# Optimization experiments

Measured on AMD Instinct MI355X. Metric: run time of the kernel, lower is better.

Reference implementation:

```python
import jax, jax.numpy as jnp
import numpy as np

D_MODEL = 1024
N_HEADS = 16
HEAD_DIM = D_MODEL // N_HEADS
ROPE_BASE = 10000.0


def setup_inputs() -> dict:
    key = jax.random.key(0)
    ks = jax.random.split(key, 9)
    s = 0.02
    inp = {
        "x": jax.random.normal(ks[0], (2, 2048, D_MODEL), dtype=jnp.float32),
        "Wq": jax.random.normal(ks[1], (D_MODEL, D_MODEL), dtype=jnp.float32) * s,
        "bq": jnp.zeros((D_MODEL,), dtype=jnp.float32),
        "Wk": jax.random.normal(ks[2], (D_MODEL, D_MODEL), dtype=jnp.float32) * s,
        "bk": jnp.zeros((D_MODEL,), dtype=jnp.float32),
        "Wv": jax.random.normal(ks[3], (D_MODEL, D_MODEL), dtype=jnp.float32) * s,
        "bv": jnp.zeros((D_MODEL,), dtype=jnp.float32),
        "Wo": jax.random.normal(ks[4], (D_MODEL, D_MODEL), dtype=jnp.float32) * s,
        "bo": jnp.zeros((D_MODEL,), dtype=jnp.float32),
    }
    return inp


def _rope_cos_sin(T, head_dim, dtype):
    inv_freq = 1.0 / (ROPE_BASE ** (jnp.arange(0, head_dim, 2, dtype=jnp.float32) / head_dim))
    pos = jnp.arange(T, dtype=jnp.float32)
    freqs = jnp.outer(pos, inv_freq)              # [T, head_dim/2]
    emb = jnp.concatenate([freqs, freqs], axis=-1)  # [T, head_dim]
    return jnp.cos(emb).astype(dtype), jnp.sin(emb).astype(dtype)


def _rotate_half(x):
    x1, x2 = jnp.split(x, 2, axis=-1)
    return jnp.concatenate([-x2, x1], axis=-1)


def reference(x, Wq, bq, Wk, bk, Wv, bv, Wo, bo):
    B, T, _ = x.shape
    H, Dh = N_HEADS, HEAD_DIM
    # projections (torch Linear: x @ W.T + b)
    q = (x @ Wq.T + bq).reshape(B, T, H, Dh).transpose(0, 2, 1, 3)  # [B,H,T,Dh]
    k = (x @ Wk.T + bk).reshape(B, T, H, Dh).transpose(0, 2, 1, 3)
    v = (x @ Wv.T + bv).reshape(B, T, H, Dh).transpose(0, 2, 1, 3)
    cos, sin = _rope_cos_sin(T, Dh, x.dtype)  # [T, Dh]
    cos = cos[None, None]
    sin = sin[None, None]
    q = q * cos + _rotate_half(q) * sin
    k = k * cos + _rotate_half(k) * sin
    scale = 1.0 / jnp.sqrt(jnp.asarray(Dh, dtype=x.dtype))
    attn = jnp.einsum("bhqd,bhkd->bhqk", q, k) * scale
    attn = jax.nn.softmax(attn, axis=-1)
    out = jnp.einsum("bhqk,bhkd->bhqd", attn, v)  # [B,H,T,Dh]
    out = out.transpose(0, 2, 1, 3).reshape(B, T, H * Dh)
    return out @ Wo.T + bo
```

## Files before the change

### kernel.cpp

```cpp
#include <hip/hip_runtime.h>
#include <hip/hip_bf16.h>
#include <cstdint>

#define D_MODEL 1024
#define NHEADS 16
#define HDIM 64
#define SEQ 2048
#define NBATCH 2
#define BT (NBATCH * SEQ)

typedef short bf16x8 __attribute__((ext_vector_type(8)));
typedef float f32x4 __attribute__((ext_vector_type(4)));
typedef unsigned short u16;
typedef unsigned int u32;

__device__ inline u16 f2bf(float f) {
    union { float f; u32 u; } x;
    x.f = f;
    u32 r = (x.u + 0x7fffu + ((x.u >> 16) & 1u)) >> 16;
    return (u16)r;
}

__device__ inline u32 pack2bf(float a, float b) {
    union { __hip_bfloat162 h; u32 u; } c;
    c.h = __float22bfloat162_rn(float2{a, b});
    return c.u;
}

__device__ inline float bf2f(u16 v) {
    union { u32 u; float f; } x;
    x.u = ((u32)v) << 16;
    return x.f;
}

__device__ inline void async_copy16(const u16* g, u16* l) {
    __builtin_amdgcn_global_load_lds((const __attribute__((address_space(1))) void*)g,
                                     (__attribute__((address_space(3))) void*)l, 16, 0, 0);
}

__device__ inline void permswap32(u32& a, u32& b) {
    asm("v_permlane32_swap_b32 %0, %1" : "+v"(a), "+v"(b));
}
__device__ inline void permswap16(u32& a, u32& b) {
    asm("v_permlane16_swap_b32 %0, %1" : "+v"(a), "+v"(b));
}

#define X4 (BT * D_MODEL / 4)
#define W4 (D_MODEL * D_MODEL / 4)
#define ROPE_N (SEQ * 32)

__global__ void prep_kernel(const float* __restrict__ x,
                            const float* __restrict__ wq, const float* __restrict__ wk,
                            const float* __restrict__ wv, const float* __restrict__ wo,
                            u16* __restrict__ xb,
                            u16* __restrict__ dq, u16* __restrict__ dk,
                            u16* __restrict__ dv, u16* __restrict__ dow,
                            float2* __restrict__ csT) {
    int idx = blockIdx.x * blockDim.x + threadIdx.x;
    if (idx < X4) {
        float4 v = ((const float4*)x)[idx];
        ushort4 o;
        o.x = f2bf(v.x); o.y = f2bf(v.y); o.z = f2bf(v.z); o.w = f2bf(v.w);
        ((ushort4*)xb)[idx] = o;
    } else if (idx < X4 + 4 * W4) {
        int j = idx - X4;
        int w = j >> 18, i = j & (W4 - 1);
        const float* s = (w == 0) ? wq : (w == 1) ? wk : (w == 2) ? wv : wo;
        u16* d = (w == 0) ? dq : (w == 1) ? dk : (w == 2) ? dv : dow;
        float4 v = ((const float4*)s)[i];
        ushort4 o;
        o.x = f2bf(v.x); o.y = f2bf(v.y); o.z = f2bf(v.z); o.w = f2bf(v.w);
        ((ushort4*)d)[i] = o;
    } else {
        int j = idx - (X4 + 4 * W4);
        if (j < ROPE_N) {
            int t = j >> 5, dm = j & 31;
            float invf = exp2f(-(float)dm * (13.287712379549449f / 32.0f));
            float ang = (float)t * invf;
            float s, c;
            sincosf(ang, &s, &c);
            csT[t * 32 + dm] = float2{c, s};
        }
    }
}

__device__ inline void gemm_tile_core(const u16* __restrict__ A, const u16* __restrict__ Bw,
                                      int blkM, int blkN,
                                      u16* Asmem, u16* Bsmem, f32x4 acc[4][4]) {
    const int tid = threadIdx.x;
    const int lane = tid & 63;
    const int wave = tid >> 6;
    const int waveM = wave >> 1, waveN = wave & 1;
    const int quad = lane >> 4, l16 = lane & 15;

    const int srow = tid >> 2;
    const int scol = (tid & 3) << 3;
    const u16* Ag0 = A + (size_t)(blkM * 128 + srow) * D_MODEL + scol;
    const u16* Ag1 = Ag0 + (size_t)64 * D_MODEL;
    const u16* Bg0 = Bw + (size_t)(blkN * 128 + srow) * D_MODEL + scol;
    const u16* Bg1 = Bg0 + (size_t)64 * D_MODEL;
    u16* Al0 = Asmem + srow * 32 + scol;
    u16* Al1 = Al0 + 64 * 32;
    u16* Bl0 = Bsmem + srow * 32 + scol;
    u16* Bl1 = Bl0 + 64 * 32;

    for (int k0 = 0; k0 < D_MODEL; k0 += 32) {
        __syncthreads();
        async_copy16(Ag0 + k0, Al0);
        async_copy16(Ag1 + k0, Al1);
        async_copy16(Bg0 + k0, Bl0);
        async_copy16(Bg1 + k0, Bl1);
        __syncthreads();
        bf16x8 af[4], bfr[4];
#pragma unroll
        for (int mt = 0; mt < 4; ++mt)
            af[mt] = *(const bf16x8*)&Asmem[(waveM * 64 + mt * 16 + l16) * 32 + quad * 8];
#pragma unroll
        for (int nt = 0; nt < 4; ++nt)
            bfr[nt] = *(const bf16x8*)&Bsmem[(waveN * 64 + nt * 16 + l16) * 32 + quad * 8];
#pragma unroll
        for (int mt = 0; mt < 4; ++mt)
#pragma unroll
            for (int nt = 0; nt < 4; ++nt)
                acc[mt][nt] = __builtin_amdgcn_mfma_f32_16x16x32_bf16(af[mt], bfr[nt], acc[mt][nt], 0, 0, 0);
    }
}

#define QSCALE 0.1803368801111204f
#define VPAD 132

__global__ __launch_bounds__(256) void gemm_qkv_kernel(
    const u16* __restrict__ xb,
    const u16* __restrict__ wqb, const u16* __restrict__ wkb, const u16* __restrict__ wvb,
    const float* __restrict__ bq, const float* __restrict__ bk, const float* __restrict__ bv,
    const float2* __restrict__ csT,
    u16* __restrict__ Qb, u16* __restrict__ Kb, u16* __restrict__ VTb) {
    __shared__ __align__(16) u16 smem[128 * VPAD];
    u16* Asmem = smem;
    u16* Bsmem = smem + 128 * 32;

    const int z = blockIdx.z;
    const u16* Bw = (z == 0) ? wqb : (z == 1) ? wkb : wvb;
    const float* bias = (z == 0) ? bq : (z == 1) ? bk : bv;

    f32x4 acc[4][4];
#pragma unroll
    for (int mt = 0; mt < 4; ++mt)
#pragma unroll
        for (int nt = 0; nt < 4; ++nt)
            acc[mt][nt] = (f32x4){0.f, 0.f, 0.f, 0.f};

    gemm_tile_core(xb, Bw, blockIdx.x, blockIdx.y, Asmem, Bsmem, acc);

    const int tid = threadIdx.x;
    const int lane = tid & 63, wave = tid >> 6;
    const int waveM = wave >> 1, waveN = wave & 1;
    const int quad = lane >> 4, l16 = lane & 15;
    const int gm0 = blockIdx.x * 128 + waveM * 64 + quad * 4;
    const int gn0 = blockIdx.y * 128 + waveN * 64 + l16;

    float bvv[4];
#pragma unroll
    for (int nt = 0; nt < 4; ++nt) bvv[nt] = bias[gn0 + nt * 16];
#pragma unroll
    for (int mt = 0; mt < 4; ++mt)
#pragma unroll
        for (int nt = 0; nt < 4; ++nt)
#pragma unroll
            for (int r = 0; r < 4; ++r) acc[mt][nt][r] += bvv[nt];

    if (z < 2) {
        u16* dst = (z == 0) ? Qb : Kb;
        const float post = (z == 0) ? QSCALE : 1.0f;
        const int h = 2 * blockIdx.y + waveN;
#pragma unroll
        for (int mt = 0; mt < 4; ++mt) {
#pragma unroll
            for (int r = 0; r < 4; ++r) {
                int gm = gm0 + mt * 16 + r;
                int t = gm & (SEQ - 1), b = gm >> 11;
                float2 cs0 = csT[t * 32 + l16];
                float2 cs1 = csT[t * 32 + 16 + l16];
                float a0 = acc[mt][0][r], a1 = acc[mt][1][r];
                float a2 = acc[mt][2][r], a3 = acc[mt][3][r];
                size_t base = ((size_t)(b * NHEADS + h) * SEQ + t) * HDIM;
                dst[base + l16]      = f2bf((a0 * cs0.x - a2 * cs0.y) * post);
                dst[base + l16 + 16] = f2bf((a1 * cs1.x - a3 * cs1.y) * post);
                dst[base + l16 + 32] = f2bf((a2 * cs0.x + a0 * cs0.y) * post);
                dst[base + l16 + 48] = f2bf((a3 * cs1.x + a1 * cs1.y) * post);
            }
        }
    } else {
        __syncthreads();
#pragma unroll
        for (int mt = 0; mt < 4; ++mt) {
            int t_local = waveM * 64 + mt * 16 + quad * 4;
#pragma unroll
            for (int nt = 0; nt < 4; ++nt) {
                int n_local = waveN * 64 + nt * 16 + l16;
                uint2 w;
                w.x = pack2bf(acc[mt][nt][0], acc[mt][nt][1]);
                w.y = pack2bf(acc[mt][nt][2], acc[mt][nt][3]);
                *(uint2*)&smem[n_local * VPAD + t_local] = w;
            }
        }
        __syncthreads();
        const int row = tid >> 1;
        const int hc = (tid & 1) * 64;
        const int n_g = blockIdx.y * 128 + row;
        const int h = n_g >> 6, d = n_g & 63;
        const int b = (blockIdx.x * 128) >> 11;
        const int t0 = ((blockIdx.x * 128) & (SEQ - 1)) + hc;
        u16* dst = &VTb[((size_t)(b * NHEADS + h) * HDIM + d) * SEQ + t0];
        const u16* src = &smem[row * VPAD + hc];
#pragma unroll
        for (int j = 0; j < 8; ++j)
            *(int4*)&dst[j * 8] = *(const int4*)&src[j * 8];
    }
}

#define LPAD 72

__global__ __launch_bounds__(256, 2) void flash_kernel(
    const u16* __restrict__ Qb, const u16* __restrict__ Kb, const u16* __restrict__ VTb,
    u16* __restrict__ Po0, u16* __restrict__ Po1, float* __restrict__ Ls) {
    __shared__ __align__(16) u16 Ks[2][64 * LPAD];
    __shared__ __align__(16) u16 VTs[2][64 * LPAD];

    const int tid = threadIdx.x;
    const int wave = tid >> 6, lane = tid & 63;
    const int quad = lane >> 4, l16 = lane & 15;
    const int bh = blockIdx.y;
    const int hf = blockIdx.z;
    const u16* Qh = Qb + (size_t)bh * SEQ * HDIM;
    const u16* Kh = Kb + ((size_t)bh * SEQ + hf * (SEQ / 2)) * HDIM;
    const u16* Vh = VTb + (size_t)bh * HDIM * SEQ + hf * (SEQ / 2);
    const int qblk = blockIdx.x * 256 + wave * 64;

    bf16x8 aq[4][2];
#pragma unroll
    for (int nt2 = 0; nt2 < 4; ++nt2)
#pragma unroll
        for (int ks = 0; ks < 2; ++ks)
            aq[nt2][ks] = *(const bf16x8*)&Qh[(qblk + nt2 * 16 + l16) * HDIM + ks * 32 + quad * 8];

    f32x4 o[4][4];
    float lsum[4] = {0.f, 0.f, 0.f, 0.f};
#pragma unroll
    for (int mt2 = 0; mt2 < 4; ++mt2)
#pragma unroll
        for (int nt = 0; nt < 4; ++nt) o[mt2][nt] = (f32x4){0.f, 0.f, 0.f, 0.f};

    const int lr = tid >> 2;
    const int lc = (tid & 3) * 16;
    const u16* Kg = Kh + (size_t)lr * HDIM + lc;
    const u16* Vg = Vh + (size_t)lr * SEQ + lc;
    const int sidx = lr * LPAD + lc;

    uint4 ka, kc, va, vc;
    ka = *(const uint4*)&Kg[0];
    kc = *(const uint4*)&Kg[8];
    va = *(const uint4*)&Vg[0];
    vc = *(const uint4*)&Vg[8];
    *(uint4*)&Ks[0][sidx] = ka;
    *(uint4*)&Ks[0][sidx + 8] = kc;
    *(uint4*)&VTs[0][sidx] = va;
    *(uint4*)&VTs[0][sidx + 8] = vc;
    ka = *(const uint4*)&Kg[(size_t)64 * HDIM];
    kc = *(const uint4*)&Kg[(size_t)64 * HDIM + 8];
    va = *(const uint4*)&Vg[64];
    vc = *(const uint4*)&Vg[64 + 8];
    __syncthreads();

#pragma unroll 2
    for (int it = 0; it < 16; ++it) {
        const int cur = it & 1;
        if (it < 15) {
            *(uint4*)&Ks[cur ^ 1][sidx] = ka;
            *(uint4*)&Ks[cur ^ 1][sidx + 8] = kc;
            *(uint4*)&VTs[cur ^ 1][sidx] = va;
            *(uint4*)&VTs[cur ^ 1][sidx + 8] = vc;
        }
        if (it < 14) {
            ka = *(const uint4*)&Kg[(size_t)(it + 2) * 64 * HDIM];
            kc = *(const uint4*)&Kg[(size_t)(it + 2) * 64 * HDIM + 8];
            va = *(const uint4*)&Vg[(it + 2) * 64];
            vc = *(const uint4*)&Vg[(it + 2) * 64 + 8];
        }
        const u16* Ksc = Ks[cur];
        const u16* Vsc = VTs[cur];

        f32x4 sacc[4][4];
#pragma unroll
        for (int mt = 0; mt < 4; ++mt)
#pragma unroll
            for (int nt2 = 0; nt2 < 4; ++nt2) sacc[mt][nt2] = (f32x4){0.f, 0.f, 0.f, 0.f};
#pragma unroll
        for (int ks = 0; ks < 2; ++ks) {
            bf16x8 kf[4];
#pragma unroll
            for (int mt = 0; mt < 4; ++mt)
                kf[mt] = *(const bf16x8*)&Ksc[(mt * 16 + l16) * LPAD + ks * 32 + quad * 8];
#pragma unroll
            for (int mt = 0; mt < 4; ++mt)
#pragma unroll
                for (int nt2 = 0; nt2 < 4; ++nt2)
                    sacc[mt][nt2] = __builtin_amdgcn_mfma_f32_16x16x32_bf16(kf[mt], aq[nt2][ks], sacc[mt][nt2], 0, 0, 0);
        }

        u32 pq[4][2][4];
#pragma unroll
        for (int nt2 = 0; nt2 < 4; ++nt2) {
            u32 w[4][2];
#pragma unroll
            for (int mt = 0; mt < 4; ++mt) {
                float p0 = __builtin_amdgcn_exp2f(sacc[mt][nt2][0]);
                float p1 = __builtin_amdgcn_exp2f(sacc[mt][nt2][1]);
                float p2 = __builtin_amdgcn_exp2f(sacc[mt][nt2][2]);
                float p3 = __builtin_amdgcn_exp2f(sacc[mt][nt2][3]);
                lsum[nt2] += (p0 + p1) + (p2 + p3);
                w[mt][0] = pack2bf(p0, p1);
                w[mt][1] = pack2bf(p2, p3);
            }
#pragma unroll
            for (int ks = 0; ks < 2; ++ks)
#pragma unroll
                for (int h = 0; h < 2; ++h) {
                    u32 a = w[2 * ks][h], b = w[2 * ks + 1][h];
                    permswap32(a, b);
                    permswap16(a, b);
                    pq[nt2][ks][h] = a;
                    pq[nt2][ks][2 + h] = b;
                }
        }

#pragma unroll
        for (int ks = 0; ks < 2; ++ks) {
            bf16x8 vf[4];
#pragma unroll
            for (int nt = 0; nt < 4; ++nt)
                vf[nt] = *(const bf16x8*)&Vsc[(nt * 16 + l16) * LPAD + ks * 32 + quad * 8];
#pragma unroll
            for (int mt2 = 0; mt2 < 4; ++mt2) {
                union { u32 u[4]; bf16x8 v; } pf;
                pf.u[0] = pq[mt2][ks][0];
                pf.u[1] = pq[mt2][ks][1];
                pf.u[2] = pq[mt2][ks][2];
                pf.u[3] = pq[mt2][ks][3];
#pragma unroll
                for (int nt = 0; nt < 4; ++nt)
                    o[mt2][nt] = __builtin_amdgcn_mfma_f32_16x16x32_bf16(pf.v, vf[nt], o[mt2][nt], 0, 0, 0);
            }
        }
        __syncthreads();
    }

#pragma unroll
    for (int nt2 = 0; nt2 < 4; ++nt2) {
        lsum[nt2] += __shfl_xor(lsum[nt2], 16, 64);
        lsum[nt2] += __shfl_xor(lsum[nt2], 32, 64);
    }

    const int b = bh >> 4, h = bh & 15;
    u16* dst = hf ? Po1 : Po0;
#pragma unroll
    for (int mt2 = 0; mt2 < 4; ++mt2) {
#pragma unroll
        for (int nt = 0; nt < 4; ++nt) {
            int d = nt * 16 + l16;
#pragma unroll
            for (int r = 0; r < 4; ++r) {
                int q = qblk + mt2 * 16 + quad * 4 + r;
                dst[((size_t)(b * SEQ + q)) * D_MODEL + h * HDIM + d] = f2bf(o[mt2][nt][r]);
            }
        }
    }
    if (quad == 0) {
#pragma unroll
        for (int nt2 = 0; nt2 < 4; ++nt2) {
            int q = qblk + nt2 * 16 + l16;
            Ls[hf * (32 * SEQ) + bh * SEQ + q] = lsum[nt2];
        }
    }
}

__global__ __launch_bounds__(256) void gemm_out_kernel(
    const u16* __restrict__ Po0, const u16* __restrict__ Po1, const float* __restrict__ Ls,
    const u16* __restrict__ wob, const float* __restrict__ bo, float* __restrict__ dout) {
    __shared__ __align__(16) u16 Asmem[64 * 32];
    __shared__ __align__(16) u16 Bsmem[128 * 32];

    const int tid = threadIdx.x;
    const int lane = tid & 63, wave = tid >> 6;
    const int waveM = wave >> 1, waveN = wave & 1;
    const int quad = lane >> 4, l16 = lane & 15;

    f32x4 acc[2][4];
#pragma unroll
    for (int mt = 0; mt < 2; ++mt)
#pragma unroll
        for (int nt = 0; nt < 4; ++nt) acc[mt][nt] = (f32x4){0.f, 0.f, 0.f, 0.f};

    const int srow = tid >> 2;
    const int scol = (tid & 3) << 3;
    const int q = blockIdx.x * 64 + srow;
    const int b = q >> 11, t = q & (SEQ - 1);
    const size_t arow = (size_t)q * D_MODEL + scol;
    const u16* Bg0 = wob + (size_t)(blockIdx.y * 128 + srow) * D_MODEL + scol;
    const u16* Bg1 = Bg0 + (size_t)64 * D_MODEL;
    u16* Al = Asmem + srow * 32 + scol;
    u16* Bl0 = Bsmem + srow * 32 + scol;
    u16* Bl1 = Bl0 + 64 * 32;

    float rinvh[NHEADS];
    {
        const int bhq0 = b * NHEADS * SEQ + t;
#pragma unroll
        for (int h = 0; h < NHEADS; ++h) {
            int bhq = bhq0 + h * SEQ;
            rinvh[h] = 1.0f / (Ls[bhq] + Ls[32 * SEQ + bhq]);
        }
    }

    uint4 A0 = *(const uint4*)&Po0[arow];
    uint4 A1 = *(const uint4*)&Po1[arow];

    for (int k0 = 0; k0 < D_MODEL; k0 += 32) {
        __syncthreads();
        float rinv = rinvh[(k0 + scol) >> 6];
        const u16* p0 = (const u16*)&A0;
        const u16* p1 = (const u16*)&A1;
        uint4 wv;
        u32* wvp = (u32*)&wv;
#pragma unroll
        for (int j = 0; j < 4; ++j) {
            float s0 = (bf2f(p0[2 * j]) + bf2f(p1[2 * j])) * rinv;
            float s1 = (bf2f(p0[2 * j + 1]) + bf2f(p1[2 * j + 1])) * rinv;
            wvp[j] = pack2bf(s0, s1);
        }
        *(uint4*)Al = wv;
        async_copy16(Bg0 + k0, Bl0);
        async_copy16(Bg1 + k0, Bl1);
        if (k0 + 32 < D_MODEL) {
            A0 = *(const uint4*)&Po0[arow + k0 + 32];
            A1 = *(const uint4*)&Po1[arow + k0 + 32];
        }
        __syncthreads();
        bf16x8 af[2], bfr[4];
#pragma unroll
        for (int mt = 0; mt < 2; ++mt)
            af[mt] = *(const bf16x8*)&Asmem[(waveM * 32 + mt * 16 + l16) * 32 + quad * 8];
#pragma unroll
        for (int nt = 0; nt < 4; ++nt)
            bfr[nt] = *(const bf16x8*)&Bsmem[(waveN * 64 + nt * 16 + l16) * 32 + quad * 8];
#pragma unroll
        for (int mt = 0; mt < 2; ++mt)
#pragma unroll
            for (int nt = 0; nt < 4; ++nt)
                acc[mt][nt] = __builtin_amdgcn_mfma_f32_16x16x32_bf16(af[mt], bfr[nt], acc[mt][nt], 0, 0, 0);
    }

    const int gm0 = blockIdx.x * 64 + waveM * 32 + quad * 4;
    const int gn0 = blockIdx.y * 128 + waveN * 64 + l16;

    float bvv[4];
#pragma unroll
    for (int nt = 0; nt < 4; ++nt) bvv[nt] = bo[gn0 + nt * 16];
#pragma unroll
    for (int mt = 0; mt < 2; ++mt)
#pragma unroll
        for (int nt = 0; nt < 4; ++nt)
#pragma unroll
            for (int r = 0; r < 4; ++r)
                dout[(size_t)(gm0 + mt * 16 + r) * D_MODEL + gn0 + nt * 16] = acc[mt][nt][r] + bvv[nt];
}

extern "C" void kernel_launch(void* const* d_in, const int* in_sizes, int n_in,
                              void* d_out, int out_size, void* d_ws, size_t ws_size,
                              hipStream_t stream) {
    const float* x  = (const float*)d_in[0];
    const float* Wq = (const float*)d_in[1];
    const float* bq = (const float*)d_in[2];
    const float* Wk = (const float*)d_in[3];
    const float* bk = (const float*)d_in[4];
    const float* Wv = (const float*)d_in[5];
    const float* bv = (const float*)d_in[6];
    const float* Wo = (const float*)d_in[7];
    const float* bo = (const float*)d_in[8];
    float* dout = (float*)d_out;

    char* ws = (char*)d_ws;
    size_t off = 0;
    u16* xb  = (u16*)(ws + off); off += (size_t)BT * D_MODEL * 2;
    u16* wqb = (u16*)(ws + off); off += (size_t)D_MODEL * D_MODEL * 2;
    u16* wkb = (u16*)(ws + off); off += (size_t)D_MODEL * D_MODEL * 2;
    u16* wvb = (u16*)(ws + off); off += (size_t)D_MODEL * D_MODEL * 2;
    u16* wob = (u16*)(ws + off); off += (size_t)D_MODEL * D_MODEL * 2;
    u16* Qb  = (u16*)(ws + off); off += (size_t)BT * D_MODEL * 2;
    u16* Kb  = (u16*)(ws + off); off += (size_t)BT * D_MODEL * 2;
    u16* VTb = (u16*)(ws + off); off += (size_t)BT * D_MODEL * 2;
    u16* Po0 = (u16*)(ws + off); off += (size_t)BT * D_MODEL * 2;
    float2* csT = (float2*)(ws + off); off += (size_t)SEQ * 32 * 8;
    float* Ls   = (float*)(ws + off); off += (size_t)2 * 32 * SEQ * 4;
    u16* Po1 = xb;

    const int prepN = X4 + 4 * W4 + ROPE_N;
    prep_kernel<<<dim3((prepN + 255) / 256), 256, 0, stream>>>(
        x, Wq, Wk, Wv, Wo, xb, wqb, wkb, wvb, wob, csT);
    gemm_qkv_kernel<<<dim3(BT / 128, D_MODEL / 128, 3), 256, 0, stream>>>(
        xb, wqb, wkb, wvb, bq, bk, bv, csT, Qb, Kb, VTb);
    flash_kernel<<<dim3(SEQ / 256, NBATCH * NHEADS, 2), 256, 0, stream>>>(
        Qb, Kb, VTb, Po0, Po1, Ls);
    gemm_out_kernel<<<dim3(BT / 64, D_MODEL / 128), 256, 0, stream>>>(
        Po0, Po1, Ls, wob, bo, dout);
}
```

Before: 201.7 us.

## Split flash attention KV range four ways when workspace allows

The flash kernel now takes a variable KV iteration count and can split the key sequence into four chunks instead of two, writing four partial outputs and row sums. The output GEMM combines all partials before normalising. The launch bound is raised to four blocks per SM, and the 4-way path is used only if the workspace is large enough. This doubles the flash grid to raise occupancy and parallelism, at the cost of more partial-output traffic in the output GEMM and possible register pressure under the tighter launch bound.

```diff
diff --git a/kernel.cpp b/kernel.cpp
--- a/kernel.cpp
+++ b/kernel.cpp
@@ -221,9 +221,10 @@
 
 #define LPAD 72
 
-__global__ __launch_bounds__(256, 2) void flash_kernel(
+__global__ __launch_bounds__(256, 4) void flash_kernel(
     const u16* __restrict__ Qb, const u16* __restrict__ Kb, const u16* __restrict__ VTb,
-    u16* __restrict__ Po0, u16* __restrict__ Po1, float* __restrict__ Ls) {
+    u16* __restrict__ Po0, u16* __restrict__ Po1, u16* __restrict__ Po2, u16* __restrict__ Po3,
+    float* __restrict__ Ls, int iters) {
     __shared__ __align__(16) u16 Ks[2][64 * LPAD];
     __shared__ __align__(16) u16 VTs[2][64 * LPAD];
 
@@ -233,8 +234,8 @@
     const int bh = blockIdx.y;
     const int hf = blockIdx.z;
     const u16* Qh = Qb + (size_t)bh * SEQ * HDIM;
-    const u16* Kh = Kb + ((size_t)bh * SEQ + hf * (SEQ / 2)) * HDIM;
-    const u16* Vh = VTb + (size_t)bh * HDIM * SEQ + hf * (SEQ / 2);
+    const u16* Kh = Kb + ((size_t)bh * SEQ + (size_t)hf * iters * 64) * HDIM;
+    const u16* Vh = VTb + (size_t)bh * HDIM * SEQ + (size_t)hf * iters * 64;
     const int qblk = blockIdx.x * 256 + wave * 64;
 
     bf16x8 aq[4][2];
@@ -273,15 +274,15 @@
     __syncthreads();
 
 #pragma unroll 2
-    for (int it = 0; it < 16; ++it) {
+    for (int it = 0; it < iters; ++it) {
         const int cur = it & 1;
-        if (it < 15) {
+        if (it < iters - 1) {
             *(uint4*)&Ks[cur ^ 1][sidx] = ka;
             *(uint4*)&Ks[cur ^ 1][sidx + 8] = kc;
             *(uint4*)&VTs[cur ^ 1][sidx] = va;
             *(uint4*)&VTs[cur ^ 1][sidx + 8] = vc;
         }
-        if (it < 14) {
+        if (it < iters - 2) {
             ka = *(const uint4*)&Kg[(size_t)(it + 2) * 64 * HDIM];
             kc = *(const uint4*)&Kg[(size_t)(it + 2) * 64 * HDIM + 8];
             va = *(const uint4*)&Vg[(it + 2) * 64];
@@ -362,7 +363,7 @@
     }
 
     const int b = bh >> 4, h = bh & 15;
-    u16* dst = hf ? Po1 : Po0;
+    u16* dst = (hf == 0) ? Po0 : (hf == 1) ? Po1 : (hf == 2) ? Po2 : Po3;
 #pragma unroll
     for (int mt2 = 0; mt2 < 4; ++mt2) {
 #pragma unroll
@@ -385,8 +386,11 @@
 }
 
 __global__ __launch_bounds__(256) void gemm_out_kernel(
-    const u16* __restrict__ Po0, const u16* __restrict__ Po1, const float* __restrict__ Ls,
-    const u16* __restrict__ wob, const float* __restrict__ bo, float* __restrict__ dout) {
+    const u16* __restrict__ Po0, const u16* __restrict__ Po1,
+    const u16* __restrict__ Po2, const u16* __restrict__ Po3,
+    const float* __restrict__ Ls,
+    const u16* __restrict__ wob, const float* __restrict__ bo, float* __restrict__ dout,
+    int nsplit) {
     __shared__ __align__(16) u16 Asmem[64 * 32];
     __shared__ __align__(16) u16 Bsmem[128 * 32];
 
@@ -418,25 +422,38 @@
 #pragma unroll
         for (int h = 0; h < NHEADS; ++h) {
             int bhq = bhq0 + h * SEQ;
-            rinvh[h] = 1.0f / (Ls[bhq] + Ls[32 * SEQ + bhq]);
+            float s = Ls[bhq] + Ls[32 * SEQ + bhq];
+            if (nsplit == 4) s += Ls[2 * 32 * SEQ + bhq] + Ls[3 * 32 * SEQ + bhq];
+            rinvh[h] = 1.0f / s;
         }
     }
 
     uint4 A0 = *(const uint4*)&Po0[arow];
     uint4 A1 = *(const uint4*)&Po1[arow];
+    uint4 A2, A3;
+    if (nsplit == 4) {
+        A2 = *(const uint4*)&Po2[arow];
+        A3 = *(const uint4*)&Po3[arow];
+    }
 
     for (int k0 = 0; k0 < D_MODEL; k0 += 32) {
         __syncthreads();
         float rinv = rinvh[(k0 + scol) >> 6];
         const u16* p0 = (const u16*)&A0;
         const u16* p1 = (const u16*)&A1;
+        const u16* p2 = (const u16*)&A2;
+        const u16* p3 = (const u16*)&A3;
         uint4 wv;
         u32* wvp = (u32*)&wv;
 #pragma unroll
         for (int j = 0; j < 4; ++j) {
-            float s0 = (bf2f(p0[2 * j]) + bf2f(p1[2 * j])) * rinv;
-            float s1 = (bf2f(p0[2 * j + 1]) + bf2f(p1[2 * j + 1])) * rinv;
-            wvp[j] = pack2bf(s0, s1);
+            float s0 = bf2f(p0[2 * j]) + bf2f(p1[2 * j]);
+            float s1 = bf2f(p0[2 * j + 1]) + bf2f(p1[2 * j + 1]);
+            if (nsplit == 4) {
+                s0 += bf2f(p2[2 * j]) + bf2f(p3[2 * j]);
+                s1 += bf2f(p2[2 * j + 1]) + bf2f(p3[2 * j + 1]);
+            }
+            wvp[j] = pack2bf(s0 * rinv, s1 * rinv);
         }
         *(uint4*)Al = wv;
         async_copy16(Bg0 + k0, Bl0);
@@ -444,6 +461,10 @@
         if (k0 + 32 < D_MODEL) {
             A0 = *(const uint4*)&Po0[arow + k0 + 32];
             A1 = *(const uint4*)&Po1[arow + k0 + 32];
+            if (nsplit == 4) {
+                A2 = *(const uint4*)&Po2[arow + k0 + 32];
+                A3 = *(const uint4*)&Po3[arow + k0 + 32];
+            }
         }
         __syncthreads();
         bf16x8 af[2], bfr[4];
@@ -501,16 +522,25 @@
     u16* VTb = (u16*)(ws + off); off += (size_t)BT * D_MODEL * 2;
     u16* Po0 = (u16*)(ws + off); off += (size_t)BT * D_MODEL * 2;
     float2* csT = (float2*)(ws + off); off += (size_t)SEQ * 32 * 8;
-    float* Ls   = (float*)(ws + off); off += (size_t)2 * 32 * SEQ * 4;
+    float* Ls   = (float*)(ws + off); off += (size_t)4 * 32 * SEQ * 4;
     u16* Po1 = xb;
+
+    int S = 2;
+    u16* Po2 = Po0;
+    u16* Po3 = Po0;
+    if (ws_size >= off + 2 * (size_t)BT * D_MODEL * 2) {
+        Po2 = (u16*)(ws + off); off += (size_t)BT * D_MODEL * 2;
+        Po3 = (u16*)(ws + off); off += (size_t)BT * D_MODEL * 2;
+        S = 4;
+    }
 
     const int prepN = X4 + 4 * W4 + ROPE_N;
     prep_kernel<<<dim3((prepN + 255) / 256), 256, 0, stream>>>(
         x, Wq, Wk, Wv, Wo, xb, wqb, wkb, wvb, wob, csT);
     gemm_qkv_kernel<<<dim3(BT / 128, D_MODEL / 128, 3), 256, 0, stream>>>(
         xb, wqb, wkb, wvb, bq, bk, bv, csT, Qb, Kb, VTb);
-    flash_kernel<<<dim3(SEQ / 256, NBATCH * NHEADS, 2), 256, 0, stream>>>(
-        Qb, Kb, VTb, Po0, Po1, Ls);
+    flash_kernel<<<dim3(SEQ / 256, NBATCH * NHEADS, S), 256, 0, stream>>>(
+        Qb, Kb, VTb, Po0, Po1, Po2, Po3, Ls, (SEQ / 64) / S);
     gemm_out_kernel<<<dim3(BT / 64, D_MODEL / 128), 256, 0, stream>>>(
-        Po0, Po1, Ls, wob, bo, dout);
-}
+        Po0, Po1, Po2, Po3, Ls, wob, bo, dout, S);
+}
```

After: 417.6 us. 2.07x slower.

## Double-buffer QKV GEMM k-loop with register prefetch of next tiles

Applied to the files above, without the earlier changes.

Replaces the single-buffered async-copy k-loop in the QKV projection GEMM with a two-stage LDS double buffer. Global loads for the tile two steps ahead are staged in registers while MFMAs run on the current buffer, and there is now one barrier per iteration instead of two. This aims to hide global-load latency behind compute, at the cost of more registers and twice the LDS for the A/B tiles, which still fits in the existing shared array.

```diff
diff --git a/kernel.cpp b/kernel.cpp
--- a/kernel.cpp
+++ b/kernel.cpp
@@ -84,48 +84,6 @@
     }
 }
 
-__device__ inline void gemm_tile_core(const u16* __restrict__ A, const u16* __restrict__ Bw,
-                                      int blkM, int blkN,
-                                      u16* Asmem, u16* Bsmem, f32x4 acc[4][4]) {
-    const int tid = threadIdx.x;
-    const int lane = tid & 63;
-    const int wave = tid >> 6;
-    const int waveM = wave >> 1, waveN = wave & 1;
-    const int quad = lane >> 4, l16 = lane & 15;
-
-    const int srow = tid >> 2;
-    const int scol = (tid & 3) << 3;
-    const u16* Ag0 = A + (size_t)(blkM * 128 + srow) * D_MODEL + scol;
-    const u16* Ag1 = Ag0 + (size_t)64 * D_MODEL;
-    const u16* Bg0 = Bw + (size_t)(blkN * 128 + srow) * D_MODEL + scol;
-    const u16* Bg1 = Bg0 + (size_t)64 * D_MODEL;
-    u16* Al0 = Asmem + srow * 32 + scol;
-    u16* Al1 = Al0 + 64 * 32;
-    u16* Bl0 = Bsmem + srow * 32 + scol;
-    u16* Bl1 = Bl0 + 64 * 32;
-
-    for (int k0 = 0; k0 < D_MODEL; k0 += 32) {
-        __syncthreads();
-        async_copy16(Ag0 + k0, Al0);
-        async_copy16(Ag1 + k0, Al1);
-        async_copy16(Bg0 + k0, Bl0);
-        async_copy16(Bg1 + k0, Bl1);
-        __syncthreads();
-        bf16x8 af[4], bfr[4];
-#pragma unroll
-        for (int mt = 0; mt < 4; ++mt)
-            af[mt] = *(const bf16x8*)&Asmem[(waveM * 64 + mt * 16 + l16) * 32 + quad * 8];
-#pragma unroll
-        for (int nt = 0; nt < 4; ++nt)
-            bfr[nt] = *(const bf16x8*)&Bsmem[(waveN * 64 + nt * 16 + l16) * 32 + quad * 8];
-#pragma unroll
-        for (int mt = 0; mt < 4; ++mt)
-#pragma unroll
-            for (int nt = 0; nt < 4; ++nt)
-                acc[mt][nt] = __builtin_amdgcn_mfma_f32_16x16x32_bf16(af[mt], bfr[nt], acc[mt][nt], 0, 0, 0);
-    }
-}
-
 #define QSCALE 0.1803368801111204f
 #define VPAD 132
 
@@ -136,26 +94,82 @@
     const float2* __restrict__ csT,
     u16* __restrict__ Qb, u16* __restrict__ Kb, u16* __restrict__ VTb) {
     __shared__ __align__(16) u16 smem[128 * VPAD];
-    u16* Asmem = smem;
-    u16* Bsmem = smem + 128 * 32;
 
     const int z = blockIdx.z;
     const u16* Bw = (z == 0) ? wqb : (z == 1) ? wkb : wvb;
     const float* bias = (z == 0) ? bq : (z == 1) ? bk : bv;
-
-    f32x4 acc[4][4];
-#pragma unroll
-    for (int mt = 0; mt < 4; ++mt)
-#pragma unroll
-        for (int nt = 0; nt < 4; ++nt)
-            acc[mt][nt] = (f32x4){0.f, 0.f, 0.f, 0.f};
-
-    gemm_tile_core(xb, Bw, blockIdx.x, blockIdx.y, Asmem, Bsmem, acc);
 
     const int tid = threadIdx.x;
     const int lane = tid & 63, wave = tid >> 6;
     const int waveM = wave >> 1, waveN = wave & 1;
     const int quad = lane >> 4, l16 = lane & 15;
+
+    f32x4 acc[4][4];
+#pragma unroll
+    for (int mt = 0; mt < 4; ++mt)
+#pragma unroll
+        for (int nt = 0; nt < 4; ++nt)
+            acc[mt][nt] = (f32x4){0.f, 0.f, 0.f, 0.f};
+
+    const int srow = tid >> 2;
+    const int scol = (tid & 3) << 3;
+    const u16* Ag0 = xb + (size_t)(blockIdx.x * 128 + srow) * D_MODEL + scol;
+    const u16* Ag1 = Ag0 + (size_t)64 * D_MODEL;
+    const u16* Bg0 = Bw + (size_t)(blockIdx.y * 128 + srow) * D_MODEL + scol;
+    const u16* Bg1 = Bg0 + (size_t)64 * D_MODEL;
+    const int sidx = srow * 32 + scol;
+    u16* As = smem;
+    u16* Bs = smem + 8192;
+
+    uint4 a0 = *(const uint4*)&Ag0[0];
+    uint4 a1 = *(const uint4*)&Ag1[0];
+    uint4 b0 = *(const uint4*)&Bg0[0];
+    uint4 b1 = *(const uint4*)&Bg1[0];
+    *(uint4*)&As[sidx] = a0;
+    *(uint4*)&As[sidx + 2048] = a1;
+    *(uint4*)&Bs[sidx] = b0;
+    *(uint4*)&Bs[sidx + 2048] = b1;
+    a0 = *(const uint4*)&Ag0[32];
+    a1 = *(const uint4*)&Ag1[32];
+    b0 = *(const uint4*)&Bg0[32];
+    b1 = *(const uint4*)&Bg1[32];
+    __syncthreads();
+
+#pragma unroll 2
+    for (int it = 0; it < 32; ++it) {
+        const int cur = it & 1;
+        if (it < 31) {
+            u16* Ad = As + (cur ^ 1) * 4096;
+            u16* Bd = Bs + (cur ^ 1) * 4096;
+            *(uint4*)&Ad[sidx] = a0;
+            *(uint4*)&Ad[sidx + 2048] = a1;
+            *(uint4*)&Bd[sidx] = b0;
+            *(uint4*)&Bd[sidx + 2048] = b1;
+        }
+        if (it < 30) {
+            const int k = (it + 2) * 32;
+            a0 = *(const uint4*)&Ag0[k];
+            a1 = *(const uint4*)&Ag1[k];
+            b0 = *(const uint4*)&Bg0[k];
+            b1 = *(const uint4*)&Bg1[k];
+        }
+        const u16* Ac = As + cur * 4096;
+        const u16* Bc = Bs + cur * 4096;
+        bf16x8 af[4], bfr[4];
+#pragma unroll
+        for (int mt = 0; mt < 4; ++mt)
+            af[mt] = *(const bf16x8*)&Ac[(waveM * 64 + mt * 16 + l16) * 32 + quad * 8];
+#pragma unroll
+        for (int nt = 0; nt < 4; ++nt)
+            bfr[nt] = *(const bf16x8*)&Bc[(waveN * 64 + nt * 16 + l16) * 32 + quad * 8];
+#pragma unroll
+        for (int mt = 0; mt < 4; ++mt)
+#pragma unroll
+            for (int nt = 0; nt < 4; ++nt)
+                acc[mt][nt] = __builtin_amdgcn_mfma_f32_16x16x32_bf16(af[mt], bfr[nt], acc[mt][nt], 0, 0, 0);
+        __syncthreads();
+    }
+
     const int gm0 = blockIdx.x * 128 + waveM * 64 + quad * 4;
     const int gn0 = blockIdx.y * 128 + waveN * 64 + l16;
 
@@ -181,13 +195,13 @@
                 int t = gm & (SEQ - 1), b = gm >> 11;
                 float2 cs0 = csT[t * 32 + l16];
                 float2 cs1 = csT[t * 32 + 16 + l16];
-                float a0 = acc[mt][0][r], a1 = acc[mt][1][r];
-                float a2 = acc[mt][2][r], a3 = acc[mt][3][r];
+                float a0f = acc[mt][0][r], a1f = acc[mt][1][r];
+                float a2f = acc[mt][2][r], a3f = acc[mt][3][r];
                 size_t base = ((size_t)(b * NHEADS + h) * SEQ + t) * HDIM;
-                dst[base + l16]      = f2bf((a0 * cs0.x - a2 * cs0.y) * post);
-                dst[base + l16 + 16] = f2bf((a1 * cs1.x - a3 * cs1.y) * post);
-                dst[base + l16 + 32] = f2bf((a2 * cs0.x + a0 * cs0.y) * post);
-                dst[base + l16 + 48] = f2bf((a3 * cs1.x + a1 * cs1.y) * post);
+                dst[base + l16]      = f2bf((a0f * cs0.x - a2f * cs0.y) * post);
+                dst[base + l16 + 16] = f2bf((a1f * cs1.x - a3f * cs1.y) * post);
+                dst[base + l16 + 32] = f2bf((a2f * cs0.x + a0f * cs0.y) * post);
+                dst[base + l16 + 48] = f2bf((a3f * cs1.x + a1f * cs1.y) * post);
             }
         }
     } else {
```

New measurement: 204.2 us. Within noise of the previous version (+1.3%).
